# Optimization experiments

Hardware: AMD Instinct MI355X
Metric: run time of the kernel (lower is better)

Reference implementation:

```python
import jax, jax.numpy as jnp
import numpy as np
from jax import lax

INPUT_DIM = 256
OUTPUT_DIM = 128
HIDDEN_DIM = 512
BATCH = 32768
T0, T1 = 0.0, 1.0
N_STEPS = 40  # fixed-step RK4 stand-in for adaptive odeint


def setup_inputs() -> dict:
    key = jax.random.key(0)
    ks = jax.random.split(key, 10)
    s_in = 1.0 / np.sqrt(INPUT_DIM)
    s_h = 1.0 / np.sqrt(HIDDEN_DIM)
    return {
        "x": jax.random.normal(ks[0], (BATCH, INPUT_DIM), dtype=jnp.float32),
        # input_x: Linear(input_dim -> hidden_dim)
        "Wx": jax.random.uniform(ks[1], (HIDDEN_DIM, INPUT_DIM), jnp.float32, -s_in, s_in),
        "bx": jax.random.uniform(ks[2], (HIDDEN_DIM,), jnp.float32, -s_in, s_in),
        # LiquidODEFunc params: dh/dt = (-h + tanh(W h + U u + b)) / tau
        "W": jax.random.uniform(ks[3], (HIDDEN_DIM, HIDDEN_DIM), jnp.float32, -s_h, s_h),
        "U": jax.random.uniform(ks[4], (HIDDEN_DIM, HIDDEN_DIM), jnp.float32, -s_h, s_h),
        "b": jax.random.uniform(ks[5], (HIDDEN_DIM,), jnp.float32, -s_h, s_h),
        "tau": jnp.ones((HIDDEN_DIM,), dtype=jnp.float32)
             + 0.1 * jax.random.uniform(ks[6], (HIDDEN_DIM,), jnp.float32),
        # forward_head: Linear(hidden_dim -> output_dim)
        "Wf": jax.random.uniform(ks[7], (OUTPUT_DIM, HIDDEN_DIM), jnp.float32, -s_h, s_h),
        "bf": jax.random.uniform(ks[8], (OUTPUT_DIM,), jnp.float32, -s_h, s_h),
    }


def reference(x, Wx, bx, W, U, b, tau, Wf, bf):
    # x -> latent projection
    u = x @ Wx.T + bx                       # (B, H)
    # input drive U u + b is constant over the ODE solve; precompute once
    drive = u @ U.T + b                     # (B, H)
    dt = (T1 - T0) / N_STEPS

    def f(h):
        return (-h + jnp.tanh(h @ W.T + drive)) / tau

    def rk4_step(h, _):
        k1 = f(h)
        k2 = f(h + 0.5 * dt * k1)
        k3 = f(h + 0.5 * dt * k2)
        k4 = f(h + dt * k3)
        return h + (dt / 6.0) * (k1 + 2.0 * k2 + 2.0 * k3 + k4), None

    h_T, _ = lax.scan(rk4_step, u, None, length=N_STEPS)  # h0 = u_proj
    return h_T @ Wf.T + bf                   # (B, output_dim)
```

## Files before the change

### kernel.cpp

```cpp
#include <hip/hip_runtime.h>
#include <stdint.h>

#define IN_DIM 256
#define HID 512
#define OUT_DIM 128
#define BT 64
#define NSTEPS 40
#define TPB 512

typedef float f32x4 __attribute__((ext_vector_type(4)));
typedef __bf16 bf16x8 __attribute__((ext_vector_type(8)));

#define TANH_SC 2.8853900817779268f

static __device__ __forceinline__ uint32_t cvtpk(float a, float b) {
  uint32_t r;
  asm("v_cvt_pk_bf16_f32 %0, %1, %2" : "=v"(r) : "v"(a), "v"(b));
  return r;
}
static __device__ __forceinline__ float bflo(uint32_t u) {
  union { uint32_t u; float f; } v; v.u = u << 16; return v.f;
}
static __device__ __forceinline__ float bfhi(uint32_t u) {
  union { uint32_t u; float f; } v; v.u = u & 0xFFFF0000u; return v.f;
}
static __device__ __forceinline__ uint32_t pkh(float a, float b) {
  const uint16_t lo = __builtin_bit_cast(uint16_t, (_Float16)a);
  const uint16_t hi = __builtin_bit_cast(uint16_t, (_Float16)b);
  return (uint32_t)lo | ((uint32_t)hi << 16);
}
static __device__ __forceinline__ float h2lo(uint32_t u) {
  return (float)__builtin_bit_cast(_Float16, (uint16_t)(u & 0xFFFFu));
}
static __device__ __forceinline__ float h2hi(uint32_t u) {
  return (float)__builtin_bit_cast(_Float16, (uint16_t)(u >> 16));
}
static __device__ __forceinline__ float tanh_fast(float x) {
  const float e = __builtin_amdgcn_exp2f(x);
  return __builtin_fmaf(-2.0f, __builtin_amdgcn_rcpf(e + 1.0f), 1.0f);
}

static __device__ __forceinline__ int lds_ea(int m, int n) {
  return m * 1024 + ((((n >> 3) ^ (m & 15)) << 4)) + ((n & 7) << 1);
}

template <int NKSEG>
static __device__ __forceinline__ void mm_sw(const __bf16* __restrict__ Ap,
                                             const char* lds, int B1,
                                             f32x4 acc[4][4]) {
#pragma unroll 2
  for (int ks = 0; ks < NKSEG; ++ks) {
    const int ba = (B1 ^ ((ks & 3) << 6)) + ((ks >> 2) << 8);
    bf16x8 wf[4];
#pragma unroll
    for (int i = 0; i < 4; ++i)
      wf[i] = *(const bf16x8*)(Ap + (size_t)(i * NKSEG + ks) * 512);
#pragma unroll
    for (int j = 0; j < 4; ++j) {
      const bf16x8 hf = *(const bf16x8*)(lds + ba + j * 16384);
#pragma unroll
      for (int i = 0; i < 4; ++i)
        acc[i][j] = __builtin_amdgcn_mfma_f32_16x16x32_bf16(wf[i], hf,
                                                            acc[i][j], 0, 0, 0);
    }
  }
}

__global__ __launch_bounds__(TPB, 2) void liq_main(
    const float* __restrict__ x, const float* __restrict__ bx,
    const float* __restrict__ bvec, const float* __restrict__ tau,
    const float* __restrict__ bfh, const __bf16* __restrict__ Wx_p,
    const __bf16* __restrict__ U_p, const __bf16* __restrict__ W_p,
    const __bf16* __restrict__ Wf_p, float* __restrict__ out) {
  __shared__ __align__(16) char abuf[BT * 1024];
  __shared__ __align__(8) uint2 drv[16 * TPB];
  const int tid = threadIdx.x;
  const int w = tid >> 6;
  const int lane = tid & 63;
  const int l15 = lane & 15;
  const int q = lane >> 4;
  const int row0 = blockIdx.x * BT;

  const int B1 =
      l15 * 1024 + ((q ^ (l15 & 3)) << 4) + (((l15 >> 2) & 3) << 6);
  const int chunk0 = (((q >> 1) ^ (l15 & 1))) | (((l15 >> 1) & 3) << 1) |
                     ((8 * w) ^ (l15 & 8));
  const int A0 = l15 * 1024 + ((q & 1) << 3) + (chunk0 << 4);

  {
    const float4* x4 = (const float4*)(x + (size_t)row0 * IN_DIM);
#pragma unroll
    for (int it = 0; it < (BT * IN_DIM / 4) / TPB; ++it) {
      const int id = tid + it * TPB;
      const float4 v = x4[id];
      const int m = id >> 6;
      const int c = (id & 63) << 2;
      uint2 pk;
      pk.x = cvtpk(v.x, v.y);
      pk.y = cvtpk(v.z, v.w);
      *(uint2*)(abuf + lds_ea(m, c)) = pk;
    }
  }

  f32x4 it4[4];
#pragma unroll
  for (int i = 0; i < 4; ++i) {
    const float4 tv = *(const float4*)(tau + 64 * w + 16 * i + 4 * q);
    it4[i] = (f32x4){1.0f / tv.x, 1.0f / tv.y, 1.0f / tv.z, 1.0f / tv.w};
  }
  __syncthreads();

  f32x4 acc[4][4];
#pragma unroll
  for (int i = 0; i < 4; ++i) {
    const float4 b4 = *(const float4*)(bx + 64 * w + 16 * i + 4 * q);
#pragma unroll
    for (int j = 0; j < 4; ++j) acc[i][j] = (f32x4){b4.x, b4.y, b4.z, b4.w};
  }
  mm_sw<IN_DIM / 32>(Wx_p + (size_t)w * 16384 + lane * 8, abuf, B1, acc);

  uint32_t h16[32];
#pragma unroll
  for (int i = 0; i < 4; ++i)
#pragma unroll
    for (int j = 0; j < 4; ++j) {
      const int ti = i * 4 + j;
      h16[ti * 2] = pkh(acc[i][j][0], acc[i][j][1]);
      h16[ti * 2 + 1] = pkh(acc[i][j][2], acc[i][j][3]);
    }

  __syncthreads();
#pragma unroll
  for (int i = 0; i < 4; ++i)
#pragma unroll
    for (int j = 0; j < 4; ++j) {
      uint2 pk;
      pk.x = cvtpk(acc[i][j][0], acc[i][j][1]);
      pk.y = cvtpk(acc[i][j][2], acc[i][j][3]);
      *(uint2*)(abuf + ((A0 ^ (i << 5)) + j * 16384)) = pk;
    }
  __syncthreads();

#pragma unroll
  for (int i = 0; i < 4; ++i) {
    const float4 b4 = *(const float4*)(bvec + 64 * w + 16 * i + 4 * q);
#pragma unroll
    for (int j = 0; j < 4; ++j)
      acc[i][j] = (f32x4){b4.x * TANH_SC, b4.y * TANH_SC, b4.z * TANH_SC,
                          b4.w * TANH_SC};
  }
  mm_sw<HID / 32>(U_p + (size_t)w * 32768 + lane * 8, abuf, B1, acc);
#pragma unroll
  for (int i = 0; i < 4; ++i)
#pragma unroll
    for (int j = 0; j < 4; ++j) {
      uint2 pk;
      pk.x = cvtpk(acc[i][j][0], acc[i][j][1]);
      pk.y = cvtpk(acc[i][j][2], acc[i][j][3]);
      drv[(i * 4 + j) * TPB + tid] = pk;
    }

  const float dt = 1.0f / NSTEPS;
  const float hdt = 0.5f * dt;
  const float dt6 = dt / 6.0f;
  f32x4 Sp[16];
  const __bf16* Wp_base = W_p + (size_t)w * 32768 + lane * 8;

  for (int st = 0; st < NSTEPS; ++st) {
    for (int e = 0; e < 4; ++e) {
#pragma unroll
      for (int i = 0; i < 4; ++i)
#pragma unroll
        for (int j = 0; j < 4; ++j) {
          const uint2 d = drv[(i * 4 + j) * TPB + tid];
          acc[i][j] = (f32x4){bflo(d.x), bfhi(d.x), bflo(d.y), bfhi(d.y)};
        }
      mm_sw<HID / 32>(Wp_base, abuf, B1, acc);

      const float wk = (e == 1 || e == 2) ? 2.0f : 1.0f;
      const float cn = (e < 2) ? hdt : ((e == 2) ? dt : dt6);
#pragma unroll
      for (int i = 0; i < 4; ++i)
#pragma unroll
        for (int j = 0; j < 4; ++j) {
          const int ti = i * 4 + j;
          const int sa = (A0 ^ (i << 5)) + j * 16384;
          const float hc0 = h2lo(h16[ti * 2]), hc1 = h2hi(h16[ti * 2]);
          const float hc2 = h2lo(h16[ti * 2 + 1]), hc3 = h2hi(h16[ti * 2 + 1]);
          float hin[4];
          if (e == 0) {
            hin[0] = hc0; hin[1] = hc1; hin[2] = hc2; hin[3] = hc3;
          } else {
            const uint2 hb = *(const uint2*)(abuf + sa);
            hin[0] = bflo(hb.x); hin[1] = bfhi(hb.x);
            hin[2] = bflo(hb.y); hin[3] = bfhi(hb.y);
          }
          float kk[4];
          kk[0] = (tanh_fast(acc[i][j][0]) - hin[0]) * it4[i][0];
          kk[1] = (tanh_fast(acc[i][j][1]) - hin[1]) * it4[i][1];
          kk[2] = (tanh_fast(acc[i][j][2]) - hin[2]) * it4[i][2];
          kk[3] = (tanh_fast(acc[i][j][3]) - hin[3]) * it4[i][3];
          if (e == 0) {
            Sp[ti] = (f32x4){kk[0], kk[1], kk[2], kk[3]};
          } else if (e < 3) {
            Sp[ti][0] = __builtin_fmaf(wk, kk[0], Sp[ti][0]);
            Sp[ti][1] = __builtin_fmaf(wk, kk[1], Sp[ti][1]);
            Sp[ti][2] = __builtin_fmaf(wk, kk[2], Sp[ti][2]);
            Sp[ti][3] = __builtin_fmaf(wk, kk[3], Sp[ti][3]);
          }
          float n0, n1, n2, n3;
          if (e == 3) {
            n0 = __builtin_fmaf(dt6, Sp[ti][0] + kk[0], hc0);
            n1 = __builtin_fmaf(dt6, Sp[ti][1] + kk[1], hc1);
            n2 = __builtin_fmaf(dt6, Sp[ti][2] + kk[2], hc2);
            n3 = __builtin_fmaf(dt6, Sp[ti][3] + kk[3], hc3);
            h16[ti * 2] = pkh(n0, n1);
            h16[ti * 2 + 1] = pkh(n2, n3);
          } else {
            n0 = __builtin_fmaf(cn, kk[0], hc0);
            n1 = __builtin_fmaf(cn, kk[1], hc1);
            n2 = __builtin_fmaf(cn, kk[2], hc2);
            n3 = __builtin_fmaf(cn, kk[3], hc3);
          }
          acc[i][j][0] = n0; acc[i][j][1] = n1;
          acc[i][j][2] = n2; acc[i][j][3] = n3;
        }
      __syncthreads();
#pragma unroll
      for (int i = 0; i < 4; ++i)
#pragma unroll
        for (int j = 0; j < 4; ++j) {
          uint2 pk;
          pk.x = cvtpk(acc[i][j][0], acc[i][j][1]);
          pk.y = cvtpk(acc[i][j][2], acc[i][j][3]);
          *(uint2*)(abuf + ((A0 ^ (i << 5)) + j * 16384)) = pk;
        }
      __syncthreads();
    }
  }

  {
    const float4 b4 = *(const float4*)(bfh + 16 * w + 4 * q);
    f32x4 a2[4];
#pragma unroll
    for (int j = 0; j < 4; ++j) a2[j] = (f32x4){b4.x, b4.y, b4.z, b4.w};
#pragma unroll 2
    for (int ks = 0; ks < HID / 32; ++ks) {
      const bf16x8 wf =
          *(const bf16x8*)(Wf_p + (size_t)(w * 16 + ks) * 512 + lane * 8);
      const int ba = (B1 ^ ((ks & 3) << 6)) + ((ks >> 2) << 8);
#pragma unroll
      for (int j = 0; j < 4; ++j) {
        const bf16x8 hf = *(const bf16x8*)(abuf + ba + j * 16384);
        a2[j] = __builtin_amdgcn_mfma_f32_16x16x32_bf16(wf, hf, a2[j], 0, 0, 0);
      }
    }
#pragma unroll
    for (int j = 0; j < 4; ++j) {
      float4 o;
      o.x = a2[j][0]; o.y = a2[j][1]; o.z = a2[j][2]; o.w = a2[j][3];
      *(float4*)(out + (size_t)(row0 + 16 * j + l15) * OUT_DIM + 16 * w +
                 4 * q) = o;
    }
  }
}

__global__ void pack_bfrag(const float* __restrict__ src, __bf16* __restrict__ dst,
                           int K, int kslog, int total, float scale) {
  const int i = blockIdx.x * blockDim.x + threadIdx.x;
  if (i >= total) return;
  const int j = i & 7;
  const int lane = (i >> 3) & 63;
  const int rem = i >> 9;
  const int ks = rem & ((1 << kslog) - 1);
  const int nt = rem >> kslog;
  const int n = (nt << 4) + (lane & 15);
  const int k = (ks << 5) + ((lane >> 4) << 3) + j;
  dst[i] = (__bf16)(src[n * K + k] * scale);
}

extern "C" void kernel_launch(void* const* d_in, const int* in_sizes, int n_in,
                              void* d_out, int out_size, void* d_ws, size_t ws_size,
                              hipStream_t stream) {
  const float* x = (const float*)d_in[0];
  const float* Wx = (const float*)d_in[1];
  const float* bx = (const float*)d_in[2];
  const float* W = (const float*)d_in[3];
  const float* U = (const float*)d_in[4];
  const float* b = (const float*)d_in[5];
  const float* tau = (const float*)d_in[6];
  const float* Wf = (const float*)d_in[7];
  const float* bf_ = (const float*)d_in[8];
  float* out = (float*)d_out;

  char* ws = (char*)d_ws;
  __bf16* W_p = (__bf16*)(ws + 0);
  __bf16* U_p = (__bf16*)(ws + (512 * 1024));
  __bf16* Wx_p = (__bf16*)(ws + (1024 * 1024));
  __bf16* Wf_p = (__bf16*)(ws + (1280 * 1024));

  pack_bfrag<<<(HID * HID) / 256, 256, 0, stream>>>(W, W_p, HID, 4, HID * HID,
                                                    TANH_SC);
  pack_bfrag<<<(HID * HID) / 256, 256, 0, stream>>>(U, U_p, HID, 4, HID * HID,
                                                    TANH_SC);
  pack_bfrag<<<(HID * IN_DIM) / 256, 256, 0, stream>>>(Wx, Wx_p, IN_DIM, 3,
                                                       HID * IN_DIM, 1.0f);
  pack_bfrag<<<(OUT_DIM * HID) / 256, 256, 0, stream>>>(Wf, Wf_p, HID, 4,
                                                        OUT_DIM * HID, 1.0f);

  liq_main<<<32768 / BT, TPB, 0, stream>>>(x, bx, b, tau, bf_, Wx_p, U_p, W_p,
                                           Wf_p, out);
}
```

Before: 2.965 ms.

## Use 1024-thread blocks with double-buffered LDS state and register-held drive

Doubles threads per block so each wave owns 32 hidden units instead of 64, which halves the per-wave accumulator and state registers. The drive term moves from LDS into packed registers, and the RK4 weighted-sum accumulator is kept in bf16 to save registers. The LDS state is now ping-ponged between two buffers, so each stage needs one barrier instead of two. This risks extra precision loss from bf16 accumulation of the RK4 sum and needs more LDS per block, which may limit occupancy.

```diff
diff --git a/kernel.cpp b/kernel.cpp
--- a/kernel.cpp
+++ b/kernel.cpp
@@ -6,7 +6,7 @@
 #define OUT_DIM 128
 #define BT 64
 #define NSTEPS 40
-#define TPB 512
+#define TPB 1024
 
 typedef float f32x4 __attribute__((ext_vector_type(4)));
 typedef __bf16 bf16x8 __attribute__((ext_vector_type(8)));
@@ -47,33 +47,31 @@
 template <int NKSEG>
 static __device__ __forceinline__ void mm_sw(const __bf16* __restrict__ Ap,
                                              const char* lds, int B1,
-                                             f32x4 acc[4][4]) {
+                                             f32x4 acc[2][4]) {
 #pragma unroll 2
   for (int ks = 0; ks < NKSEG; ++ks) {
     const int ba = (B1 ^ ((ks & 3) << 6)) + ((ks >> 2) << 8);
-    bf16x8 wf[4];
-#pragma unroll
-    for (int i = 0; i < 4; ++i)
-      wf[i] = *(const bf16x8*)(Ap + (size_t)(i * NKSEG + ks) * 512);
+    const bf16x8 wf0 = *(const bf16x8*)(Ap + (size_t)ks * 512);
+    const bf16x8 wf1 = *(const bf16x8*)(Ap + (size_t)(NKSEG + ks) * 512);
 #pragma unroll
     for (int j = 0; j < 4; ++j) {
       const bf16x8 hf = *(const bf16x8*)(lds + ba + j * 16384);
-#pragma unroll
-      for (int i = 0; i < 4; ++i)
-        acc[i][j] = __builtin_amdgcn_mfma_f32_16x16x32_bf16(wf[i], hf,
-                                                            acc[i][j], 0, 0, 0);
-    }
-  }
-}
-
-__global__ __launch_bounds__(TPB, 2) void liq_main(
+      acc[0][j] = __builtin_amdgcn_mfma_f32_16x16x32_bf16(wf0, hf, acc[0][j],
+                                                          0, 0, 0);
+      acc[1][j] = __builtin_amdgcn_mfma_f32_16x16x32_bf16(wf1, hf, acc[1][j],
+                                                          0, 0, 0);
+    }
+  }
+}
+
+__global__ __launch_bounds__(TPB, 4) void liq_main(
     const float* __restrict__ x, const float* __restrict__ bx,
     const float* __restrict__ bvec, const float* __restrict__ tau,
     const float* __restrict__ bfh, const __bf16* __restrict__ Wx_p,
     const __bf16* __restrict__ U_p, const __bf16* __restrict__ W_p,
     const __bf16* __restrict__ Wf_p, float* __restrict__ out) {
-  __shared__ __align__(16) char abuf[BT * 1024];
-  __shared__ __align__(8) uint2 drv[16 * TPB];
+  __shared__ __align__(16) char bufA[BT * 1024];
+  __shared__ __align__(16) char bufB[BT * 1024];
   const int tid = threadIdx.x;
   const int w = tid >> 6;
   const int lane = tid & 63;
@@ -83,8 +81,8 @@
 
   const int B1 =
       l15 * 1024 + ((q ^ (l15 & 3)) << 4) + (((l15 >> 2) & 3) << 6);
-  const int chunk0 = (((q >> 1) ^ (l15 & 1))) | (((l15 >> 1) & 3) << 1) |
-                     ((8 * w) ^ (l15 & 8));
+  const int chunk0 = ((q >> 1) ^ (l15 & 1)) | (((l15 >> 1) & 1) << 1) |
+                     ((4 * w) ^ (l15 & 12));
   const int A0 = l15 * 1024 + ((q & 1) << 3) + (chunk0 << 4);
 
   {
@@ -98,30 +96,30 @@
       uint2 pk;
       pk.x = cvtpk(v.x, v.y);
       pk.y = cvtpk(v.z, v.w);
-      *(uint2*)(abuf + lds_ea(m, c)) = pk;
-    }
-  }
-
-  f32x4 it4[4];
-#pragma unroll
-  for (int i = 0; i < 4; ++i) {
-    const float4 tv = *(const float4*)(tau + 64 * w + 16 * i + 4 * q);
+      *(uint2*)(bufA + lds_ea(m, c)) = pk;
+    }
+  }
+
+  f32x4 it4[2];
+#pragma unroll
+  for (int i = 0; i < 2; ++i) {
+    const float4 tv = *(const float4*)(tau + 32 * w + 16 * i + 4 * q);
     it4[i] = (f32x4){1.0f / tv.x, 1.0f / tv.y, 1.0f / tv.z, 1.0f / tv.w};
   }
   __syncthreads();
 
-  f32x4 acc[4][4];
-#pragma unroll
-  for (int i = 0; i < 4; ++i) {
-    const float4 b4 = *(const float4*)(bx + 64 * w + 16 * i + 4 * q);
+  f32x4 acc[2][4];
+#pragma unroll
+  for (int i = 0; i < 2; ++i) {
+    const float4 b4 = *(const float4*)(bx + 32 * w + 16 * i + 4 * q);
 #pragma unroll
     for (int j = 0; j < 4; ++j) acc[i][j] = (f32x4){b4.x, b4.y, b4.z, b4.w};
   }
-  mm_sw<IN_DIM / 32>(Wx_p + (size_t)w * 16384 + lane * 8, abuf, B1, acc);
-
-  uint32_t h16[32];
-#pragma unroll
-  for (int i = 0; i < 4; ++i)
+  mm_sw<IN_DIM / 32>(Wx_p + (size_t)w * 8192 + lane * 8, bufA, B1, acc);
+
+  uint32_t h16[16];
+#pragma unroll
+  for (int i = 0; i < 2; ++i)
 #pragma unroll
     for (int j = 0; j < 4; ++j) {
       const int ti = i * 4 + j;
@@ -129,58 +127,61 @@
       h16[ti * 2 + 1] = pkh(acc[i][j][2], acc[i][j][3]);
     }
 
-  __syncthreads();
-#pragma unroll
-  for (int i = 0; i < 4; ++i)
+#pragma unroll
+  for (int i = 0; i < 2; ++i)
 #pragma unroll
     for (int j = 0; j < 4; ++j) {
       uint2 pk;
       pk.x = cvtpk(acc[i][j][0], acc[i][j][1]);
       pk.y = cvtpk(acc[i][j][2], acc[i][j][3]);
-      *(uint2*)(abuf + ((A0 ^ (i << 5)) + j * 16384)) = pk;
+      *(uint2*)(bufB + ((A0 ^ (i << 5)) + j * 16384)) = pk;
     }
   __syncthreads();
 
 #pragma unroll
-  for (int i = 0; i < 4; ++i) {
-    const float4 b4 = *(const float4*)(bvec + 64 * w + 16 * i + 4 * q);
+  for (int i = 0; i < 2; ++i) {
+    const float4 b4 = *(const float4*)(bvec + 32 * w + 16 * i + 4 * q);
 #pragma unroll
     for (int j = 0; j < 4; ++j)
       acc[i][j] = (f32x4){b4.x * TANH_SC, b4.y * TANH_SC, b4.z * TANH_SC,
                           b4.w * TANH_SC};
   }
-  mm_sw<HID / 32>(U_p + (size_t)w * 32768 + lane * 8, abuf, B1, acc);
-#pragma unroll
-  for (int i = 0; i < 4; ++i)
+  mm_sw<HID / 32>(U_p + (size_t)w * 16384 + lane * 8, bufB, B1, acc);
+  uint32_t drvp[16];
+#pragma unroll
+  for (int i = 0; i < 2; ++i)
 #pragma unroll
     for (int j = 0; j < 4; ++j) {
-      uint2 pk;
-      pk.x = cvtpk(acc[i][j][0], acc[i][j][1]);
-      pk.y = cvtpk(acc[i][j][2], acc[i][j][3]);
-      drv[(i * 4 + j) * TPB + tid] = pk;
+      const int ti = i * 4 + j;
+      drvp[ti * 2] = cvtpk(acc[i][j][0], acc[i][j][1]);
+      drvp[ti * 2 + 1] = cvtpk(acc[i][j][2], acc[i][j][3]);
     }
 
   const float dt = 1.0f / NSTEPS;
   const float hdt = 0.5f * dt;
   const float dt6 = dt / 6.0f;
-  f32x4 Sp[16];
-  const __bf16* Wp_base = W_p + (size_t)w * 32768 + lane * 8;
+  uint32_t Sp[16];
+  const __bf16* Wp_base = W_p + (size_t)w * 16384 + lane * 8;
+
+  const char* rb = bufB;
+  char* wb = bufA;
 
   for (int st = 0; st < NSTEPS; ++st) {
     for (int e = 0; e < 4; ++e) {
 #pragma unroll
-      for (int i = 0; i < 4; ++i)
+      for (int i = 0; i < 2; ++i)
 #pragma unroll
         for (int j = 0; j < 4; ++j) {
-          const uint2 d = drv[(i * 4 + j) * TPB + tid];
-          acc[i][j] = (f32x4){bflo(d.x), bfhi(d.x), bflo(d.y), bfhi(d.y)};
+          const int ti = i * 4 + j;
+          acc[i][j] = (f32x4){bflo(drvp[ti * 2]), bfhi(drvp[ti * 2]),
+                              bflo(drvp[ti * 2 + 1]), bfhi(drvp[ti * 2 + 1])};
         }
-      mm_sw<HID / 32>(Wp_base, abuf, B1, acc);
+      mm_sw<HID / 32>(Wp_base, rb, B1, acc);
 
       const float wk = (e == 1 || e == 2) ? 2.0f : 1.0f;
-      const float cn = (e < 2) ? hdt : ((e == 2) ? dt : dt6);
-#pragma unroll
-      for (int i = 0; i < 4; ++i)
+      const float cn = (e < 2) ? hdt : dt;
+#pragma unroll
+      for (int i = 0; i < 2; ++i)
 #pragma unroll
         for (int j = 0; j < 4; ++j) {
           const int ti = i * 4 + j;
@@ -191,7 +192,7 @@
           if (e == 0) {
             hin[0] = hc0; hin[1] = hc1; hin[2] = hc2; hin[3] = hc3;
           } else {
-            const uint2 hb = *(const uint2*)(abuf + sa);
+            const uint2 hb = *(const uint2*)(rb + sa);
             hin[0] = bflo(hb.x); hin[1] = bfhi(hb.x);
             hin[2] = bflo(hb.y); hin[3] = bfhi(hb.y);
           }
@@ -200,67 +201,68 @@
           kk[1] = (tanh_fast(acc[i][j][1]) - hin[1]) * it4[i][1];
           kk[2] = (tanh_fast(acc[i][j][2]) - hin[2]) * it4[i][2];
           kk[3] = (tanh_fast(acc[i][j][3]) - hin[3]) * it4[i][3];
+          float n0, n1, n2, n3;
           if (e == 0) {
-            Sp[ti] = (f32x4){kk[0], kk[1], kk[2], kk[3]};
-          } else if (e < 3) {
-            Sp[ti][0] = __builtin_fmaf(wk, kk[0], Sp[ti][0]);
-            Sp[ti][1] = __builtin_fmaf(wk, kk[1], Sp[ti][1]);
-            Sp[ti][2] = __builtin_fmaf(wk, kk[2], Sp[ti][2]);
-            Sp[ti][3] = __builtin_fmaf(wk, kk[3], Sp[ti][3]);
-          }
-          float n0, n1, n2, n3;
-          if (e == 3) {
-            n0 = __builtin_fmaf(dt6, Sp[ti][0] + kk[0], hc0);
-            n1 = __builtin_fmaf(dt6, Sp[ti][1] + kk[1], hc1);
-            n2 = __builtin_fmaf(dt6, Sp[ti][2] + kk[2], hc2);
-            n3 = __builtin_fmaf(dt6, Sp[ti][3] + kk[3], hc3);
-            h16[ti * 2] = pkh(n0, n1);
-            h16[ti * 2 + 1] = pkh(n2, n3);
-          } else {
+            Sp[ti * 2] = cvtpk(kk[0], kk[1]);
+            Sp[ti * 2 + 1] = cvtpk(kk[2], kk[3]);
             n0 = __builtin_fmaf(cn, kk[0], hc0);
             n1 = __builtin_fmaf(cn, kk[1], hc1);
             n2 = __builtin_fmaf(cn, kk[2], hc2);
             n3 = __builtin_fmaf(cn, kk[3], hc3);
+          } else if (e < 3) {
+            const float s0 = __builtin_fmaf(wk, kk[0], bflo(Sp[ti * 2]));
+            const float s1 = __builtin_fmaf(wk, kk[1], bfhi(Sp[ti * 2]));
+            const float s2 = __builtin_fmaf(wk, kk[2], bflo(Sp[ti * 2 + 1]));
+            const float s3 = __builtin_fmaf(wk, kk[3], bfhi(Sp[ti * 2 + 1]));
+            Sp[ti * 2] = cvtpk(s0, s1);
+            Sp[ti * 2 + 1] = cvtpk(s2, s3);
+            n0 = __builtin_fmaf(cn, kk[0], hc0);
+            n1 = __builtin_fmaf(cn, kk[1], hc1);
+            n2 = __builtin_fmaf(cn, kk[2], hc2);
+            n3 = __builtin_fmaf(cn, kk[3], hc3);
+          } else {
+            n0 = __builtin_fmaf(dt6, bflo(Sp[ti * 2]) + kk[0], hc0);
+            n1 = __builtin_fmaf(dt6, bfhi(Sp[ti * 2]) + kk[1], hc1);
+            n2 = __builtin_fmaf(dt6, bflo(Sp[ti * 2 + 1]) + kk[2], hc2);
+            n3 = __builtin_fmaf(dt6, bfhi(Sp[ti * 2 + 1]) + kk[3], hc3);
+            h16[ti * 2] = pkh(n0, n1);
+            h16[ti * 2 + 1] = pkh(n2, n3);
           }
-          acc[i][j][0] = n0; acc[i][j][1] = n1;
-          acc[i][j][2] = n2; acc[i][j][3] = n3;
+          uint2 pk;
+          pk.x = cvtpk(n0, n1);
+          pk.y = cvtpk(n2, n3);
+          *(uint2*)(wb + sa) = pk;
         }
       __syncthreads();
-#pragma unroll
-      for (int i = 0; i < 4; ++i)
-#pragma unroll
-        for (int j = 0; j < 4; ++j) {
-          uint2 pk;
-          pk.x = cvtpk(acc[i][j][0], acc[i][j][1]);
-          pk.y = cvtpk(acc[i][j][2], acc[i][j][3]);
-          *(uint2*)(abuf + ((A0 ^ (i << 5)) + j * 16384)) = pk;
-        }
-      __syncthreads();
+      const char* t = rb; rb = wb; wb = (char*)t;
     }
   }
 
   {
-    const float4 b4 = *(const float4*)(bfh + 16 * w + 4 * q);
-    f32x4 a2[4];
-#pragma unroll
-    for (int j = 0; j < 4; ++j) a2[j] = (f32x4){b4.x, b4.y, b4.z, b4.w};
+    const int ct = w & 7;
+    const int j0 = (w >> 3) * 2;
+    const float4 b4 = *(const float4*)(bfh + 16 * ct + 4 * q);
+    f32x4 a2[2];
+#pragma unroll
+    for (int jj = 0; jj < 2; ++jj) a2[jj] = (f32x4){b4.x, b4.y, b4.z, b4.w};
 #pragma unroll 2
     for (int ks = 0; ks < HID / 32; ++ks) {
       const bf16x8 wf =
-          *(const bf16x8*)(Wf_p + (size_t)(w * 16 + ks) * 512 + lane * 8);
+          *(const bf16x8*)(Wf_p + (size_t)(ct * 16 + ks) * 512 + lane * 8);
       const int ba = (B1 ^ ((ks & 3) << 6)) + ((ks >> 2) << 8);
 #pragma unroll
-      for (int j = 0; j < 4; ++j) {
-        const bf16x8 hf = *(const bf16x8*)(abuf + ba + j * 16384);
-        a2[j] = __builtin_amdgcn_mfma_f32_16x16x32_bf16(wf, hf, a2[j], 0, 0, 0);
+      for (int jj = 0; jj < 2; ++jj) {
+        const bf16x8 hf = *(const bf16x8*)(rb + ba + (j0 + jj) * 16384);
+        a2[jj] =
+            __builtin_amdgcn_mfma_f32_16x16x32_bf16(wf, hf, a2[jj], 0, 0, 0);
       }
     }
 #pragma unroll
-    for (int j = 0; j < 4; ++j) {
+    for (int jj = 0; jj < 2; ++jj) {
       float4 o;
-      o.x = a2[j][0]; o.y = a2[j][1]; o.z = a2[j][2]; o.w = a2[j][3];
-      *(float4*)(out + (size_t)(row0 + 16 * j + l15) * OUT_DIM + 16 * w +
-                 4 * q) = o;
+      o.x = a2[jj][0]; o.y = a2[jj][1]; o.z = a2[jj][2]; o.w = a2[jj][3];
+      *(float4*)(out + (size_t)(row0 + 16 * (j0 + jj) + l15) * OUT_DIM +
+                 16 * ct + 4 * q) = o;
     }
   }
 }
```

Result: slower. 4.093 ms (+38.1%).

## Double-buffer the LDS state tile to drop a barrier per RK4 stage

Applied to the files above, without the earlier changes.

Replaces the single LDS activation buffer plus the LDS drive buffer with two ping-pong activation buffers. Each stage reads the current state from one buffer and writes the next stage input into the other, so only one __syncthreads is needed per stage instead of two. The drive term, the RK4 partial sum and the inverse tau are now held in registers as packed bf16 rather than fp32 or in LDS, which keeps register pressure within bounds. Storing the RK4 accumulator and 1/tau in bf16 loses precision and could change numerical accuracy.

```diff
diff --git a/kernel.cpp b/kernel.cpp
--- a/kernel.cpp
+++ b/kernel.cpp
@@ -72,8 +72,8 @@
     const float* __restrict__ bfh, const __bf16* __restrict__ Wx_p,
     const __bf16* __restrict__ U_p, const __bf16* __restrict__ W_p,
     const __bf16* __restrict__ Wf_p, float* __restrict__ out) {
-  __shared__ __align__(16) char abuf[BT * 1024];
-  __shared__ __align__(8) uint2 drv[16 * TPB];
+  __shared__ __align__(16) char bufA[BT * 1024];
+  __shared__ __align__(16) char bufB[BT * 1024];
   const int tid = threadIdx.x;
   const int w = tid >> 6;
   const int lane = tid & 63;
@@ -98,15 +98,16 @@
       uint2 pk;
       pk.x = cvtpk(v.x, v.y);
       pk.y = cvtpk(v.z, v.w);
-      *(uint2*)(abuf + lds_ea(m, c)) = pk;
-    }
-  }
-
-  f32x4 it4[4];
+      *(uint2*)(bufA + lds_ea(m, c)) = pk;
+    }
+  }
+
+  uint32_t itp[8];
 #pragma unroll
   for (int i = 0; i < 4; ++i) {
     const float4 tv = *(const float4*)(tau + 64 * w + 16 * i + 4 * q);
-    it4[i] = (f32x4){1.0f / tv.x, 1.0f / tv.y, 1.0f / tv.z, 1.0f / tv.w};
+    itp[i * 2] = cvtpk(1.0f / tv.x, 1.0f / tv.y);
+    itp[i * 2 + 1] = cvtpk(1.0f / tv.z, 1.0f / tv.w);
   }
   __syncthreads();
 
@@ -117,7 +118,7 @@
 #pragma unroll
     for (int j = 0; j < 4; ++j) acc[i][j] = (f32x4){b4.x, b4.y, b4.z, b4.w};
   }
-  mm_sw<IN_DIM / 32>(Wx_p + (size_t)w * 16384 + lane * 8, abuf, B1, acc);
+  mm_sw<IN_DIM / 32>(Wx_p + (size_t)w * 16384 + lane * 8, bufA, B1, acc);
 
   uint32_t h16[32];
 #pragma unroll
@@ -129,7 +130,6 @@
       h16[ti * 2 + 1] = pkh(acc[i][j][2], acc[i][j][3]);
     }
 
-  __syncthreads();
 #pragma unroll
   for (int i = 0; i < 4; ++i)
 #pragma unroll
@@ -137,7 +137,7 @@
       uint2 pk;
       pk.x = cvtpk(acc[i][j][0], acc[i][j][1]);
       pk.y = cvtpk(acc[i][j][2], acc[i][j][3]);
-      *(uint2*)(abuf + ((A0 ^ (i << 5)) + j * 16384)) = pk;
+      *(uint2*)(bufB + ((A0 ^ (i << 5)) + j * 16384)) = pk;
     }
   __syncthreads();
 
@@ -149,22 +149,25 @@
       acc[i][j] = (f32x4){b4.x * TANH_SC, b4.y * TANH_SC, b4.z * TANH_SC,
                           b4.w * TANH_SC};
   }
-  mm_sw<HID / 32>(U_p + (size_t)w * 32768 + lane * 8, abuf, B1, acc);
+  mm_sw<HID / 32>(U_p + (size_t)w * 32768 + lane * 8, bufB, B1, acc);
+  uint32_t drvp[32];
 #pragma unroll
   for (int i = 0; i < 4; ++i)
 #pragma unroll
     for (int j = 0; j < 4; ++j) {
-      uint2 pk;
-      pk.x = cvtpk(acc[i][j][0], acc[i][j][1]);
-      pk.y = cvtpk(acc[i][j][2], acc[i][j][3]);
-      drv[(i * 4 + j) * TPB + tid] = pk;
+      const int ti = i * 4 + j;
+      drvp[ti * 2] = cvtpk(acc[i][j][0], acc[i][j][1]);
+      drvp[ti * 2 + 1] = cvtpk(acc[i][j][2], acc[i][j][3]);
     }
 
   const float dt = 1.0f / NSTEPS;
   const float hdt = 0.5f * dt;
   const float dt6 = dt / 6.0f;
-  f32x4 Sp[16];
+  uint32_t Sp[32];
   const __bf16* Wp_base = W_p + (size_t)w * 32768 + lane * 8;
+
+  const char* rb = bufB;
+  char* wb = bufA;
 
   for (int st = 0; st < NSTEPS; ++st) {
     for (int e = 0; e < 4; ++e) {
@@ -172,13 +175,14 @@
       for (int i = 0; i < 4; ++i)
 #pragma unroll
         for (int j = 0; j < 4; ++j) {
-          const uint2 d = drv[(i * 4 + j) * TPB + tid];
-          acc[i][j] = (f32x4){bflo(d.x), bfhi(d.x), bflo(d.y), bfhi(d.y)};
+          const int ti = i * 4 + j;
+          acc[i][j] = (f32x4){bflo(drvp[ti * 2]), bfhi(drvp[ti * 2]),
+                              bflo(drvp[ti * 2 + 1]), bfhi(drvp[ti * 2 + 1])};
         }
-      mm_sw<HID / 32>(Wp_base, abuf, B1, acc);
+      mm_sw<HID / 32>(Wp_base, rb, B1, acc);
 
       const float wk = (e == 1 || e == 2) ? 2.0f : 1.0f;
-      const float cn = (e < 2) ? hdt : ((e == 2) ? dt : dt6);
+      const float cn = (e < 2) ? hdt : dt;
 #pragma unroll
       for (int i = 0; i < 4; ++i)
 #pragma unroll
@@ -191,51 +195,49 @@
           if (e == 0) {
             hin[0] = hc0; hin[1] = hc1; hin[2] = hc2; hin[3] = hc3;
           } else {
-            const uint2 hb = *(const uint2*)(abuf + sa);
+            const uint2 hb = *(const uint2*)(rb + sa);
             hin[0] = bflo(hb.x); hin[1] = bfhi(hb.x);
             hin[2] = bflo(hb.y); hin[3] = bfhi(hb.y);
           }
           float kk[4];
-          kk[0] = (tanh_fast(acc[i][j][0]) - hin[0]) * it4[i][0];
-          kk[1] = (tanh_fast(acc[i][j][1]) - hin[1]) * it4[i][1];
-          kk[2] = (tanh_fast(acc[i][j][2]) - hin[2]) * it4[i][2];
-          kk[3] = (tanh_fast(acc[i][j][3]) - hin[3]) * it4[i][3];
+          kk[0] = (tanh_fast(acc[i][j][0]) - hin[0]) * bflo(itp[i * 2]);
+          kk[1] = (tanh_fast(acc[i][j][1]) - hin[1]) * bfhi(itp[i * 2]);
+          kk[2] = (tanh_fast(acc[i][j][2]) - hin[2]) * bflo(itp[i * 2 + 1]);
+          kk[3] = (tanh_fast(acc[i][j][3]) - hin[3]) * bfhi(itp[i * 2 + 1]);
+          float n0, n1, n2, n3;
           if (e == 0) {
-            Sp[ti] = (f32x4){kk[0], kk[1], kk[2], kk[3]};
-          } else if (e < 3) {
-            Sp[ti][0] = __builtin_fmaf(wk, kk[0], Sp[ti][0]);
-            Sp[ti][1] = __builtin_fmaf(wk, kk[1], Sp[ti][1]);
-            Sp[ti][2] = __builtin_fmaf(wk, kk[2], Sp[ti][2]);
-            Sp[ti][3] = __builtin_fmaf(wk, kk[3], Sp[ti][3]);
-          }
-          float n0, n1, n2, n3;
-          if (e == 3) {
-            n0 = __builtin_fmaf(dt6, Sp[ti][0] + kk[0], hc0);
-            n1 = __builtin_fmaf(dt6, Sp[ti][1] + kk[1], hc1);
-            n2 = __builtin_fmaf(dt6, Sp[ti][2] + kk[2], hc2);
-            n3 = __builtin_fmaf(dt6, Sp[ti][3] + kk[3], hc3);
-            h16[ti * 2] = pkh(n0, n1);
-            h16[ti * 2 + 1] = pkh(n2, n3);
-          } else {
+            Sp[ti * 2] = cvtpk(kk[0], kk[1]);
+            Sp[ti * 2 + 1] = cvtpk(kk[2], kk[3]);
             n0 = __builtin_fmaf(cn, kk[0], hc0);
             n1 = __builtin_fmaf(cn, kk[1], hc1);
             n2 = __builtin_fmaf(cn, kk[2], hc2);
             n3 = __builtin_fmaf(cn, kk[3], hc3);
+          } else if (e < 3) {
+            const float s0 = __builtin_fmaf(wk, kk[0], bflo(Sp[ti * 2]));
+            const float s1 = __builtin_fmaf(wk, kk[1], bfhi(Sp[ti * 2]));
+            const float s2 = __builtin_fmaf(wk, kk[2], bflo(Sp[ti * 2 + 1]));
+            const float s3 = __builtin_fmaf(wk, kk[3], bfhi(Sp[ti * 2 + 1]));
+            Sp[ti * 2] = cvtpk(s0, s1);
+            Sp[ti * 2 + 1] = cvtpk(s2, s3);
+            n0 = __builtin_fmaf(cn, kk[0], hc0);
+            n1 = __builtin_fmaf(cn, kk[1], hc1);
+            n2 = __builtin_fmaf(cn, kk[2], hc2);
+            n3 = __builtin_fmaf(cn, kk[3], hc3);
+          } else {
+            n0 = __builtin_fmaf(dt6, bflo(Sp[ti * 2]) + kk[0], hc0);
+            n1 = __builtin_fmaf(dt6, bfhi(Sp[ti * 2]) + kk[1], hc1);
+            n2 = __builtin_fmaf(dt6, bflo(Sp[ti * 2 + 1]) + kk[2], hc2);
+            n3 = __builtin_fmaf(dt6, bfhi(Sp[ti * 2 + 1]) + kk[3], hc3);
+            h16[ti * 2] = pkh(n0, n1);
+            h16[ti * 2 + 1] = pkh(n2, n3);
           }
-          acc[i][j][0] = n0; acc[i][j][1] = n1;
-          acc[i][j][2] = n2; acc[i][j][3] = n3;
+          uint2 pk;
+          pk.x = cvtpk(n0, n1);
+          pk.y = cvtpk(n2, n3);
+          *(uint2*)(wb + sa) = pk;
         }
       __syncthreads();
-#pragma unroll
-      for (int i = 0; i < 4; ++i)
-#pragma unroll
-        for (int j = 0; j < 4; ++j) {
-          uint2 pk;
-          pk.x = cvtpk(acc[i][j][0], acc[i][j][1]);
-          pk.y = cvtpk(acc[i][j][2], acc[i][j][3]);
-          *(uint2*)(abuf + ((A0 ^ (i << 5)) + j * 16384)) = pk;
-        }
-      __syncthreads();
+      const char* t = rb; rb = wb; wb = (char*)t;
     }
   }
 
@@ -251,7 +253,7 @@
       const int ba = (B1 ^ ((ks & 3) << 6)) + ((ks >> 2) << 8);
 #pragma unroll
       for (int j = 0; j < 4; ++j) {
-        const bf16x8 hf = *(const bf16x8*)(abuf + ba + j * 16384);
+        const bf16x8 hf = *(const bf16x8*)(rb + ba + j * 16384);
         a2[j] = __builtin_amdgcn_mfma_f32_16x16x32_bf16(wf, hf, a2[j], 0, 0, 0);
       }
     }
```

Measured after the change: 7.718 ms. 2.6x slower.

## Move drive term to global memory and double-buffer hidden state in LDS

Applied to the files above, without the earlier changes.

Adds a kernel variant that stores the constant bf16 drive term in a per-block global workspace instead of LDS. The freed LDS holds two hidden-state buffers that ping-pong, so each RK4 stage writes the next stage input to the other buffer and needs only one barrier per stage instead of a read/write hazard barrier pair. The cost is extra global/L2 traffic to reload the drive each stage (64KB per block per stage). The old LDS kernel remains as a fallback when the workspace is too small, and the final-stage coefficient expression is simplified.

```diff
diff --git a/kernel.cpp b/kernel.cpp
--- a/kernel.cpp
+++ b/kernel.cpp
@@ -66,7 +66,208 @@
   }
 }
 
-__global__ __launch_bounds__(TPB, 2) void liq_main(
+__global__ __launch_bounds__(TPB, 2) void liq_main_g(
+    const float* __restrict__ x, const float* __restrict__ bx,
+    const float* __restrict__ bvec, const float* __restrict__ tau,
+    const float* __restrict__ bfh, const __bf16* __restrict__ Wx_p,
+    const __bf16* __restrict__ U_p, const __bf16* __restrict__ W_p,
+    const __bf16* __restrict__ Wf_p, char* __restrict__ drvg_base,
+    float* __restrict__ out) {
+  __shared__ __align__(16) char bufA[BT * 1024];
+  __shared__ __align__(16) char bufB[BT * 1024];
+  const int tid = threadIdx.x;
+  const int w = tid >> 6;
+  const int lane = tid & 63;
+  const int l15 = lane & 15;
+  const int q = lane >> 4;
+  const int row0 = blockIdx.x * BT;
+  char* drvg = drvg_base + (size_t)blockIdx.x * 65536;
+
+  const int B1 =
+      l15 * 1024 + ((q ^ (l15 & 3)) << 4) + (((l15 >> 2) & 3) << 6);
+  const int chunk0 = (((q >> 1) ^ (l15 & 1))) | (((l15 >> 1) & 3) << 1) |
+                     ((8 * w) ^ (l15 & 8));
+  const int A0 = l15 * 1024 + ((q & 1) << 3) + (chunk0 << 4);
+
+  {
+    const float4* x4 = (const float4*)(x + (size_t)row0 * IN_DIM);
+#pragma unroll
+    for (int it = 0; it < (BT * IN_DIM / 4) / TPB; ++it) {
+      const int id = tid + it * TPB;
+      const float4 v = x4[id];
+      const int m = id >> 6;
+      const int c = (id & 63) << 2;
+      uint2 pk;
+      pk.x = cvtpk(v.x, v.y);
+      pk.y = cvtpk(v.z, v.w);
+      *(uint2*)(bufA + lds_ea(m, c)) = pk;
+    }
+  }
+
+  f32x4 it4[4];
+#pragma unroll
+  for (int i = 0; i < 4; ++i) {
+    const float4 tv = *(const float4*)(tau + 64 * w + 16 * i + 4 * q);
+    it4[i] = (f32x4){1.0f / tv.x, 1.0f / tv.y, 1.0f / tv.z, 1.0f / tv.w};
+  }
+  __syncthreads();
+
+  f32x4 acc[4][4];
+#pragma unroll
+  for (int i = 0; i < 4; ++i) {
+    const float4 b4 = *(const float4*)(bx + 64 * w + 16 * i + 4 * q);
+#pragma unroll
+    for (int j = 0; j < 4; ++j) acc[i][j] = (f32x4){b4.x, b4.y, b4.z, b4.w};
+  }
+  mm_sw<IN_DIM / 32>(Wx_p + (size_t)w * 16384 + lane * 8, bufA, B1, acc);
+
+  uint32_t h16[32];
+#pragma unroll
+  for (int i = 0; i < 4; ++i)
+#pragma unroll
+    for (int j = 0; j < 4; ++j) {
+      const int ti = i * 4 + j;
+      h16[ti * 2] = pkh(acc[i][j][0], acc[i][j][1]);
+      h16[ti * 2 + 1] = pkh(acc[i][j][2], acc[i][j][3]);
+    }
+
+#pragma unroll
+  for (int i = 0; i < 4; ++i)
+#pragma unroll
+    for (int j = 0; j < 4; ++j) {
+      uint2 pk;
+      pk.x = cvtpk(acc[i][j][0], acc[i][j][1]);
+      pk.y = cvtpk(acc[i][j][2], acc[i][j][3]);
+      *(uint2*)(bufB + ((A0 ^ (i << 5)) + j * 16384)) = pk;
+    }
+  __syncthreads();
+
+#pragma unroll
+  for (int i = 0; i < 4; ++i) {
+    const float4 b4 = *(const float4*)(bvec + 64 * w + 16 * i + 4 * q);
+#pragma unroll
+    for (int j = 0; j < 4; ++j)
+      acc[i][j] = (f32x4){b4.x * TANH_SC, b4.y * TANH_SC, b4.z * TANH_SC,
+                          b4.w * TANH_SC};
+  }
+  mm_sw<HID / 32>(U_p + (size_t)w * 32768 + lane * 8, bufB, B1, acc);
+#pragma unroll
+  for (int p = 0; p < 8; ++p) {
+    const int i = p >> 1;
+    const int j0 = (p & 1) * 2;
+    uint4 d4;
+    d4.x = cvtpk(acc[i][j0][0], acc[i][j0][1]);
+    d4.y = cvtpk(acc[i][j0][2], acc[i][j0][3]);
+    d4.z = cvtpk(acc[i][j0 + 1][0], acc[i][j0 + 1][1]);
+    d4.w = cvtpk(acc[i][j0 + 1][2], acc[i][j0 + 1][3]);
+    *(uint4*)(drvg + (((p * TPB + tid)) << 4)) = d4;
+  }
+  __syncthreads();
+
+  const float dt = 1.0f / NSTEPS;
+  const float hdt = 0.5f * dt;
+  const float dt6 = dt / 6.0f;
+  f32x4 Sp[16];
+  const __bf16* Wp_base = W_p + (size_t)w * 32768 + lane * 8;
+
+  const char* rb = bufB;
+  char* wb = bufA;
+
+  for (int st = 0; st < NSTEPS; ++st) {
+    for (int e = 0; e < 4; ++e) {
+#pragma unroll
+      for (int p = 0; p < 8; ++p) {
+        const int i = p >> 1;
+        const int j0 = (p & 1) * 2;
+        const uint4 d4 = *(const uint4*)(drvg + (((p * TPB + tid)) << 4));
+        acc[i][j0] = (f32x4){bflo(d4.x), bfhi(d4.x), bflo(d4.y), bfhi(d4.y)};
+        acc[i][j0 + 1] =
+            (f32x4){bflo(d4.z), bfhi(d4.z), bflo(d4.w), bfhi(d4.w)};
+      }
+      mm_sw<HID / 32>(Wp_base, rb, B1, acc);
+
+      const float wk = (e == 1 || e == 2) ? 2.0f : 1.0f;
+      const float cn = (e < 2) ? hdt : dt;
+#pragma unroll
+      for (int i = 0; i < 4; ++i)
+#pragma unroll
+        for (int j = 0; j < 4; ++j) {
+          const int ti = i * 4 + j;
+          const int sa = (A0 ^ (i << 5)) + j * 16384;
+          const float hc0 = h2lo(h16[ti * 2]), hc1 = h2hi(h16[ti * 2]);
+          const float hc2 = h2lo(h16[ti * 2 + 1]), hc3 = h2hi(h16[ti * 2 + 1]);
+          float hin[4];
+          if (e == 0) {
+            hin[0] = hc0; hin[1] = hc1; hin[2] = hc2; hin[3] = hc3;
+          } else {
+            const uint2 hb = *(const uint2*)(rb + sa);
+            hin[0] = bflo(hb.x); hin[1] = bfhi(hb.x);
+            hin[2] = bflo(hb.y); hin[3] = bfhi(hb.y);
+          }
+          float kk[4];
+          kk[0] = (tanh_fast(acc[i][j][0]) - hin[0]) * it4[i][0];
+          kk[1] = (tanh_fast(acc[i][j][1]) - hin[1]) * it4[i][1];
+          kk[2] = (tanh_fast(acc[i][j][2]) - hin[2]) * it4[i][2];
+          kk[3] = (tanh_fast(acc[i][j][3]) - hin[3]) * it4[i][3];
+          if (e == 0) {
+            Sp[ti] = (f32x4){kk[0], kk[1], kk[2], kk[3]};
+          } else if (e < 3) {
+            Sp[ti][0] = __builtin_fmaf(wk, kk[0], Sp[ti][0]);
+            Sp[ti][1] = __builtin_fmaf(wk, kk[1], Sp[ti][1]);
+            Sp[ti][2] = __builtin_fmaf(wk, kk[2], Sp[ti][2]);
+            Sp[ti][3] = __builtin_fmaf(wk, kk[3], Sp[ti][3]);
+          }
+          float n0, n1, n2, n3;
+          if (e == 3) {
+            n0 = __builtin_fmaf(dt6, Sp[ti][0] + kk[0], hc0);
+            n1 = __builtin_fmaf(dt6, Sp[ti][1] + kk[1], hc1);
+            n2 = __builtin_fmaf(dt6, Sp[ti][2] + kk[2], hc2);
+            n3 = __builtin_fmaf(dt6, Sp[ti][3] + kk[3], hc3);
+            h16[ti * 2] = pkh(n0, n1);
+            h16[ti * 2 + 1] = pkh(n2, n3);
+          } else {
+            n0 = __builtin_fmaf(cn, kk[0], hc0);
+            n1 = __builtin_fmaf(cn, kk[1], hc1);
+            n2 = __builtin_fmaf(cn, kk[2], hc2);
+            n3 = __builtin_fmaf(cn, kk[3], hc3);
+          }
+          uint2 pk;
+          pk.x = cvtpk(n0, n1);
+          pk.y = cvtpk(n2, n3);
+          *(uint2*)(wb + sa) = pk;
+        }
+      __syncthreads();
+      const char* t = rb; rb = wb; wb = (char*)t;
+    }
+  }
+
+  {
+    const float4 b4 = *(const float4*)(bfh + 16 * w + 4 * q);
+    f32x4 a2[4];
+#pragma unroll
+    for (int j = 0; j < 4; ++j) a2[j] = (f32x4){b4.x, b4.y, b4.z, b4.w};
+#pragma unroll 2
+    for (int ks = 0; ks < HID / 32; ++ks) {
+      const bf16x8 wf =
+          *(const bf16x8*)(Wf_p + (size_t)(w * 16 + ks) * 512 + lane * 8);
+      const int ba = (B1 ^ ((ks & 3) << 6)) + ((ks >> 2) << 8);
+#pragma unroll
+      for (int j = 0; j < 4; ++j) {
+        const bf16x8 hf = *(const bf16x8*)(rb + ba + j * 16384);
+        a2[j] = __builtin_amdgcn_mfma_f32_16x16x32_bf16(wf, hf, a2[j], 0, 0, 0);
+      }
+    }
+#pragma unroll
+    for (int j = 0; j < 4; ++j) {
+      float4 o;
+      o.x = a2[j][0]; o.y = a2[j][1]; o.z = a2[j][2]; o.w = a2[j][3];
+      *(float4*)(out + (size_t)(row0 + 16 * j + l15) * OUT_DIM + 16 * w +
+                 4 * q) = o;
+    }
+  }
+}
+
+__global__ __launch_bounds__(TPB, 2) void liq_main_l(
     const float* __restrict__ x, const float* __restrict__ bx,
     const float* __restrict__ bvec, const float* __restrict__ tau,
     const float* __restrict__ bfh, const __bf16* __restrict__ Wx_p,
@@ -178,7 +379,7 @@
       mm_sw<HID / 32>(Wp_base, abuf, B1, acc);
 
       const float wk = (e == 1 || e == 2) ? 2.0f : 1.0f;
-      const float cn = (e < 2) ? hdt : ((e == 2) ? dt : dt6);
+      const float cn = (e < 2) ? hdt : dt;
 #pragma unroll
       for (int i = 0; i < 4; ++i)
 #pragma unroll
@@ -298,6 +499,8 @@
   __bf16* U_p = (__bf16*)(ws + (512 * 1024));
   __bf16* Wx_p = (__bf16*)(ws + (1024 * 1024));
   __bf16* Wf_p = (__bf16*)(ws + (1280 * 1024));
+  char* drvg = ws + (2u << 20);
+  const size_t need = (2u << 20) + (size_t)(32768 / BT) * 65536;
 
   pack_bfrag<<<(HID * HID) / 256, 256, 0, stream>>>(W, W_p, HID, 4, HID * HID,
                                                     TANH_SC);
@@ -308,6 +511,11 @@
   pack_bfrag<<<(OUT_DIM * HID) / 256, 256, 0, stream>>>(Wf, Wf_p, HID, 4,
                                                         OUT_DIM * HID, 1.0f);
 
-  liq_main<<<32768 / BT, TPB, 0, stream>>>(x, bx, b, tau, bf_, Wx_p, U_p, W_p,
-                                           Wf_p, out);
-}
+  if (ws_size >= need) {
+    liq_main_g<<<32768 / BT, TPB, 0, stream>>>(x, bx, b, tau, bf_, Wx_p, U_p,
+                                               W_p, Wf_p, drvg, out);
+  } else {
+    liq_main_l<<<32768 / BT, TPB, 0, stream>>>(x, bx, b, tau, bf_, Wx_p, U_p,
+                                               W_p, Wf_p, out);
+  }
+}
```

Result: slower. 3.087 ms (+4.1%).
